# Performance work log

Measured on AMD Instinct MI355X. Metric: run time of the kernel, lower is better.

The kernel has to match this reference:

```python
import jax, jax.numpy as jnp
import numpy as np
from jax import lax

NUM_PATCHES = 64   # FPS sample count K
PATCH_SIZE = 32    # KNN neighbors per patch


def setup_inputs() -> dict:
    key = jax.random.key(0)
    points = jax.random.normal(key, (16, 65536, 3), dtype=jnp.float32)
    return {"points": points}


def _fps(xyz, K):
    """Iterative farthest point sampling. xyz: [B,N,3] -> idx [B,K].
    Deterministic start at index 0 (reference for random_start_point)."""
    B, N, _ = xyz.shape
    start = jnp.zeros((B,), dtype=jnp.int32)
    min_d0 = jnp.full((B, N), jnp.finfo(xyz.dtype).max, xyz.dtype)

    def step(carry, _):
        min_d, last = carry
        last_pt = jnp.take_along_axis(xyz, last[:, None, None], axis=1)  # [B,1,3]
        d = jnp.sum((xyz - last_pt) ** 2, axis=-1)                       # [B,N]
        min_d = jnp.minimum(min_d, d)
        nxt = jnp.argmax(min_d, axis=1).astype(jnp.int32)
        return (min_d, nxt), last

    (_, _), idxs = lax.scan(step, (min_d0, start), None, length=K)  # [K,B]
    return jnp.transpose(idxs)  # [B,K]


def _knn_idx(centers, pts, K):
    """K nearest neighbors (sorted ascending by distance). centers [B,P,3], pts [B,N,3]."""
    c2 = jnp.sum(centers * centers, -1)[:, :, None]                 # [B,P,1]
    p2 = jnp.sum(pts * pts, -1)[:, None, :]                         # [B,1,N]
    d2 = c2 + p2 - 2.0 * jnp.einsum('bpc,bnc->bpn', centers, pts)   # [B,P,N]
    _, idx = lax.top_k(-d2, K)                                      # sorted nearest-first
    return idx


def reference(points):
    xyz = points[..., :3]
    fps_idx = _fps(xyz, NUM_PATCHES)                                  # [B,P]
    centers = jnp.take_along_axis(xyz, fps_idx[..., None], axis=1)    # [B,P,3]
    idx = _knn_idx(centers, xyz, PATCH_SIZE)                          # [B,P,K]
    patches = jax.vmap(lambda p, i: p[i])(points, idx)                # [B,P,K,C]
    patches = patches.at[..., :3].add(-centers[:, :, None, :])        # center xyz part
    return patches, centers
```

## Files before the change

### kernel.cpp

```cpp
#include <hip/hip_runtime.h>
#include <float.h>

#define BATCH 16
#define NPTS  65536
#define NP    64
#define PS    32
#define SLICES 8
#define SLICE_PTS (NPTS / SLICES)
#define CAP   192


__device__ __forceinline__ unsigned long long enc64(double d) {
    unsigned long long u = (unsigned long long)__double_as_longlong(d);
    return u ^ ((u >> 63) ? 0xFFFFFFFFFFFFFFFFull : 0x8000000000000000ull);
}
__device__ __forceinline__ unsigned enc32(float f) {
    unsigned u = __float_as_uint(f);
    return u ^ ((u >> 31) ? 0xFFFFFFFFu : 0x80000000u);
}
__device__ __forceinline__ float dec32(unsigned e) {
    unsigned u = (e & 0x80000000u) ? (e ^ 0x80000000u) : ~e;
    return __uint_as_float(u);
}

#define SENT 0xFFFFFFFFFFFFFFFFull

__global__ __launch_bounds__(256, 2)
void fps_kernel(const float* __restrict__ pts,
                float* __restrict__ centers,
                unsigned long long* __restrict__ slots)
{
#pragma clang fp contract(off)
    const int b  = blockIdx.x & 15;
    const int wg = blockIdx.x >> 4;
    const int t  = threadIdx.x;
    const float* __restrict__ P = pts + (size_t)b * NPTS * 3;

    float x[16], y[16], z[16];
    double md[16];
    const int gi0 = wg * 4096 + t;
#pragma unroll
    for (int k = 0; k < 16; ++k) {
        int i = gi0 + (k << 8);
        x[k] = P[3*i+0]; y[k] = P[3*i+1]; z[k] = P[3*i+2];
        md[k] = DBL_MAX;
    }

    double cx = (double)P[0], cy = (double)P[1], cz = (double)P[2];
    if (wg == 0 && t == 0) {
        float* c0 = centers + b * (NP*3);
        c0[0] = P[0]; c0[1] = P[1]; c0[2] = P[2];
    }

    __shared__ unsigned long long wbest[4];
    __shared__ unsigned long long skey[16];

    unsigned long long* slot_it = slots + (size_t)b * 63 * 16;

    for (int it = 0; it < NP - 1; ++it) {
        double bd = -1.0; int bi = 0;
#pragma unroll
        for (int k = 0; k < 16; ++k) {
            double dx = (double)x[k] - cx;
            double dy = (double)y[k] - cy;
            double dz = (double)z[k] - cz;
            double d  = (dx*dx + dy*dy) + dz*dz;
            double m  = fmin(md[k], d);
            md[k] = m;
            if (m > bd) { bd = m; bi = gi0 + (k << 8); }
        }
        unsigned long long db  = (unsigned long long)__double_as_longlong(bd);
        unsigned long long key = 0x8000000000000000ull
                               | (db & 0xFFFFFFFFFFFF0000ull)
                               | (unsigned long long)((~bi) & 0xFFFF);
#pragma unroll
        for (int off = 32; off > 0; off >>= 1) {
            unsigned long long o = __shfl_xor(key, off, 64);
            if (o > key) key = o;
        }
        if ((t & 63) == 0) wbest[t >> 6] = key;
        __syncthreads();
        if (t == 0) {
            unsigned long long k0 = wbest[0];
            if (wbest[1] > k0) k0 = wbest[1];
            if (wbest[2] > k0) k0 = wbest[2];
            if (wbest[3] > k0) k0 = wbest[3];
            __hip_atomic_store(slot_it + wg, k0, __ATOMIC_RELAXED, __HIP_MEMORY_SCOPE_AGENT);
        }
        if (t < 16) {
            unsigned long long v;
            v = __hip_atomic_load(slot_it + t, __ATOMIC_RELAXED, __HIP_MEMORY_SCOPE_AGENT);
            while (v == 0) {
                __builtin_amdgcn_s_sleep(1);
                v = __hip_atomic_load(slot_it + t, __ATOMIC_RELAXED, __HIP_MEMORY_SCOPE_AGENT);
            }
            skey[t] = v;
        }
        __syncthreads();
        unsigned long long bk = skey[0];
#pragma unroll
        for (int j = 1; j < 16; ++j) if (skey[j] > bk) bk = skey[j];
        int sel = (int)((~bk) & 0xFFFFull);
        cx = (double)P[3*sel+0]; cy = (double)P[3*sel+1]; cz = (double)P[3*sel+2];
        if (wg == 0 && t == 0) {
            float* c = centers + b*(NP*3) + (it+1)*3;
            c[0] = P[3*sel+0]; c[1] = P[3*sel+1]; c[2] = P[3*sel+2];
        }
        slot_it += 16;
    }
}

__global__ __launch_bounds__(256, 4)
void knn_pass(const float* __restrict__ pts,
              const float* __restrict__ centers,
              unsigned long long* __restrict__ gkeys)
{
    const int t    = threadIdx.x;
    const int lane = t & 63;
    const int wid  = t >> 6;
    const int b    = blockIdx.x & 15;
    const int w    = (blockIdx.x >> 4) & 15;
    const int s    = blockIdx.x >> 8;
    const float* __restrict__ P = pts + (size_t)b * NPTS * 3;
    const int sbase = s * SLICE_PTS;
    const float4* __restrict__ P4 = (const float4*)(P + 3 * sbase);

    float cxf[4], cyf[4], czf[4], c2f[4];
#pragma unroll
    for (int g = 0; g < 4; ++g) {
        int c = b * NP + w * 4 + g;
        cxf[g] = centers[3*c+0]; cyf[g] = centers[3*c+1]; czf[g] = centers[3*c+2];
        c2f[g] = cxf[g]*cxf[g] + cyf[g]*cyf[g] + czf[g]*czf[g];
    }

    __shared__ unsigned pool[4][512];
    __shared__ float    theta4[4];
    __shared__ int      cnt4[4];
    __shared__ unsigned idxbuf[4][CAP];

    float s0[4], s1[4];
#pragma unroll
    for (int g = 0; g < 4; ++g) { s0[g] = FLT_MAX; s1[g] = FLT_MAX; }
    {
        float4 A = P4[3*t], B = P4[3*t+1], C = P4[3*t+2];
        for (int k = 0; k < SLICE_PTS/1024; ++k) {
            int vb = ((k+1) & 7)*768 + 3*t;
            float4 An = P4[vb], Bn = P4[vb+1], Cn = P4[vb+2];
            float qx[4] = {A.x, A.w, B.z, C.y};
            float qy[4] = {A.y, B.x, B.w, C.z};
            float qz[4] = {A.z, B.y, C.x, C.w};
#pragma unroll
            for (int j = 0; j < 4; ++j) {
                float px = qx[j], py = qy[j], pz = qz[j];
                float p2 = px*px + py*py + pz*pz;
#pragma unroll
                for (int g = 0; g < 4; ++g) {
                    float dt = cxf[g]*px + cyf[g]*py + czf[g]*pz;
                    float d2 = (c2f[g] + p2) - 2.0f*dt;
                    float mx = fmaxf(d2, s0[g]);
                    s0[g] = fminf(s0[g], d2);
                    s1[g] = fminf(s1[g], mx);
                }
            }
            A = An; B = Bn; C = Cn;
        }
    }
#pragma unroll
    for (int g = 0; g < 4; ++g) {
        pool[g][t]       = enc32(s0[g]);
        pool[g][256 + t] = enc32(s1[g]);
    }
    if (t < 4) cnt4[t] = 0;
    __syncthreads();

    {
        const int g = wid;
        unsigned e[8];
#pragma unroll
        for (int j = 0; j < 8; ++j) e[j] = pool[g][lane * 8 + j];
        unsigned ans = 0;
        for (int bit = 31; bit >= 0; --bit) {
            unsigned test = ans | ((1u << bit) - 1u);
            int cnt = 0;
#pragma unroll
            for (int j = 0; j < 8; ++j)
                cnt += (int)__popcll(__ballot(e[j] <= test));
            if (cnt < 32) ans |= (1u << bit);
        }
        if (lane == 0) theta4[g] = dec32(ans) + 4.0e-3f;
    }
    __syncthreads();
    float th[4];
#pragma unroll
    for (int g = 0; g < 4; ++g) th[g] = theta4[g];

    {
        float4 A = P4[3*t], B = P4[3*t+1], C = P4[3*t+2];
        for (int k = 0; k < SLICE_PTS/1024; ++k) {
            int vb = ((k+1) & 7)*768 + 3*t;
            float4 An = P4[vb], Bn = P4[vb+1], Cn = P4[vb+2];
            float qx[4] = {A.x, A.w, B.z, C.y};
            float qy[4] = {A.y, B.x, B.w, C.z};
            float qz[4] = {A.z, B.y, C.x, C.w};
            int ib = sbase + (k << 10) + (t << 2);
#pragma unroll
            for (int j = 0; j < 4; ++j) {
                float px = qx[j], py = qy[j], pz = qz[j];
                float p2 = px*px + py*py + pz*pz;
#pragma unroll
                for (int g = 0; g < 4; ++g) {
                    float dt = cxf[g]*px + cyf[g]*py + czf[g]*pz;
                    float d2 = (c2f[g] + p2) - 2.0f*dt;
                    if (d2 <= th[g]) {
                        int pos = atomicAdd(&cnt4[g], 1);
                        if (pos < CAP) idxbuf[g][pos] = (unsigned)(ib + j);
                    }
                }
            }
            A = An; B = Bn; C = Cn;
        }
    }
    __syncthreads();

    {
        const int g = wid;
        int n = cnt4[g]; if (n > CAP) n = CAP;
        double cxd, cyd, czd, c2d;
        {
#pragma clang fp contract(off)
            cxd = (double)cxf[g]; cyd = (double)cyf[g]; czd = (double)czf[g];
            c2d = (cxd*cxd + cyd*cyd) + czd*czd;
        }
        unsigned long long rg[3];
#pragma unroll
        for (int j = 0; j < 3; ++j) {
            int p_ = lane + 64*j;
            if (p_ < n) {
                unsigned i = idxbuf[g][p_];
                double d2x;
                {
#pragma clang fp contract(off)
                    double px_ = (double)P[3*i+0];
                    double py_ = (double)P[3*i+1];
                    double pz_ = (double)P[3*i+2];
                    double p2_ = (px_*px_ + py_*py_) + pz_*pz_;
                    double dt_ = (cxd*px_ + cyd*py_) + czd*pz_;
                    d2x = (c2d + p2_) - 2.0*dt_;
                }
                rg[j] = (enc64(d2x) & 0xFFFFFFFFFFFF0000ull)
                      | (unsigned long long)(i & 0xFFFF);
            } else rg[j] = SENT;
        }
        const int c = b * NP + w * 4 + g;
        unsigned long long okey = SENT;
        for (int r = 0; r < PS; ++r) {
            unsigned long long mn = rg[0]; int mp = 0;
            if (rg[1] < mn) { mn = rg[1]; mp = 1; }
            if (rg[2] < mn) { mn = rg[2]; mp = 2; }
            unsigned long long wm = mn;
#pragma unroll
            for (int off = 32; off > 0; off >>= 1) {
                unsigned long long o = __shfl_xor(wm, off, 64);
                if (o < wm) wm = o;
            }
            if (wm == mn) {
                if (mp == 0) rg[0] = SENT;
                else if (mp == 1) rg[1] = SENT;
                else rg[2] = SENT;
            }
            if (lane == r) okey = wm;
        }
        if (lane < PS)
            gkeys[((size_t)c * SLICES + s) * PS + lane] = okey;
    }
}

__global__ __launch_bounds__(256, 4)
void knn_merge(const float* __restrict__ pts,
               const float* __restrict__ centers,
               const unsigned long long* __restrict__ gkeys,
               float* __restrict__ patches)
{
    const int lane = threadIdx.x & 63;
    const int wid  = threadIdx.x >> 6;
    const int b    = blockIdx.x & 15;
    const int grp  = blockIdx.x >> 4;
    const int c    = b * NP + grp * 4 + wid;
    const float* __restrict__ P = pts + (size_t)b * NPTS * 3;

    unsigned long long rg[4];
#pragma unroll
    for (int j = 0; j < 4; ++j)
        rg[j] = gkeys[(size_t)c * (SLICES*PS) + j*64 + lane];

    unsigned long long okey = SENT;
    for (int r = 0; r < PS; ++r) {
        unsigned long long mn = rg[0]; int mp = 0;
        if (rg[1] < mn) { mn = rg[1]; mp = 1; }
        if (rg[2] < mn) { mn = rg[2]; mp = 2; }
        if (rg[3] < mn) { mn = rg[3]; mp = 3; }
        unsigned long long wm = mn;
#pragma unroll
        for (int off = 32; off > 0; off >>= 1) {
            unsigned long long o = __shfl_xor(wm, off, 64);
            if (o < wm) wm = o;
        }
        if (wm == mn) {
            if (mp == 0) rg[0] = SENT;
            else if (mp == 1) rg[1] = SENT;
            else if (mp == 2) rg[2] = SENT;
            else rg[3] = SENT;
        }
        if (lane == r) okey = wm;
    }

    const float cx = centers[3*c+0], cy = centers[3*c+1], cz = centers[3*c+2];
    if (lane < PS) {
        int i = (int)(okey & 0xFFFFull);
        float* o = patches + (((size_t)c * PS) + lane) * 3;
        o[0] = P[3*i+0] - cx;
        o[1] = P[3*i+1] - cy;
        o[2] = P[3*i+2] - cz;
    }
}

extern "C" void kernel_launch(void* const* d_in, const int* in_sizes, int n_in,
                              void* d_out, int out_size, void* d_ws, size_t ws_size,
                              hipStream_t stream)
{
    const float* pts = (const float*)d_in[0];
    float* out      = (float*)d_out;
    float* patches  = out;
    float* centers  = out + (size_t)BATCH*NP*PS*3;

    unsigned long long* slots = (unsigned long long*)d_ws;
    unsigned long long* gkeys = (unsigned long long*)((char*)d_ws + 131072);

    (void)hipMemsetAsync(d_ws, 0, (size_t)BATCH * 63 * 16 * sizeof(unsigned long long), stream);
    fps_kernel<<<dim3(256), dim3(256), 0, stream>>>(pts, centers, slots);
    knn_pass<<<dim3(2048), dim3(256), 0, stream>>>(pts, centers, gkeys);
    knn_merge<<<dim3(256), dim3(256), 0, stream>>>(pts, centers, gkeys, patches);
}
```

Measured before the change: 260.1 us.

## Speculatively select two FPS points per iteration when the runner-up provably stays farthest

Each FPS round now tracks the top two candidates per thread, wave, block and grid. If the distance between the runner-up and the new center is at least the runner-up's own min-distance, the runner-up must be the next farthest point, so both are accepted and the next round updates min-distances against two centers. This cuts the number of grid-wide spin-wait synchronisations, which dominate the serial FPS loop. In exchange each round does extra top-2 reduction and a second slot exchange, and the acceptance test relies on truncated 48-bit distance keys, which may affect exactness on ties.

```diff
diff --git a/kernel.cpp b/kernel.cpp
--- a/kernel.cpp
+++ b/kernel.cpp
@@ -47,18 +47,21 @@
     }
 
     double cx = (double)P[0], cy = (double)P[1], cz = (double)P[2];
+    double qx = 0.0, qy = 0.0, qz = 0.0;
+    bool dual = false;
     if (wg == 0 && t == 0) {
         float* c0 = centers + b * (NP*3);
         c0[0] = P[0]; c0[1] = P[1]; c0[2] = P[2];
     }
 
-    __shared__ unsigned long long wbest[4];
-    __shared__ unsigned long long skey[16];
-
-    unsigned long long* slot_it = slots + (size_t)b * 63 * 16;
-
-    for (int it = 0; it < NP - 1; ++it) {
-        double bd = -1.0; int bi = 0;
+    __shared__ unsigned long long wk1[4], wk2[4];
+    __shared__ unsigned long long sk1[16], sk2[16];
+
+    unsigned long long* slot_it = slots + (size_t)b * 63 * 32;
+
+    int nsel = 1;
+    while (nsel < NP) {
+        double bd1 = -1.0, bd2 = -1.0; int bi1 = 0, bi2 = 0;
 #pragma unroll
         for (int k = 0; k < 16; ++k) {
             double dx = (double)x[k] - cx;
@@ -66,47 +69,99 @@
             double dz = (double)z[k] - cz;
             double d  = (dx*dx + dy*dy) + dz*dz;
             double m  = fmin(md[k], d);
+            if (dual) {
+                double ex = (double)x[k] - qx;
+                double ey = (double)y[k] - qy;
+                double ez = (double)z[k] - qz;
+                double e  = (ex*ex + ey*ey) + ez*ez;
+                m = fmin(m, e);
+            }
             md[k] = m;
-            if (m > bd) { bd = m; bi = gi0 + (k << 8); }
-        }
-        unsigned long long db  = (unsigned long long)__double_as_longlong(bd);
-        unsigned long long key = 0x8000000000000000ull
-                               | (db & 0xFFFFFFFFFFFF0000ull)
-                               | (unsigned long long)((~bi) & 0xFFFF);
+            int i = gi0 + (k << 8);
+            if (m > bd1)      { bd2 = bd1; bi2 = bi1; bd1 = m; bi1 = i; }
+            else if (m > bd2) { bd2 = m;  bi2 = i; }
+        }
+        unsigned long long k1 = 0x8000000000000000ull
+            | ((unsigned long long)__double_as_longlong(bd1) & 0xFFFFFFFFFFFF0000ull)
+            | (unsigned long long)((~bi1) & 0xFFFF);
+        unsigned long long k2 = 0x8000000000000000ull
+            | ((unsigned long long)__double_as_longlong(bd2) & 0xFFFFFFFFFFFF0000ull)
+            | (unsigned long long)((~bi2) & 0xFFFF);
+
+        unsigned long long K1 = k1;
 #pragma unroll
         for (int off = 32; off > 0; off >>= 1) {
-            unsigned long long o = __shfl_xor(key, off, 64);
-            if (o > key) key = o;
-        }
-        if ((t & 63) == 0) wbest[t >> 6] = key;
+            unsigned long long o = __shfl_xor(K1, off, 64);
+            if (o > K1) K1 = o;
+        }
+        unsigned long long K2 = (k1 == K1) ? k2 : k1;
+#pragma unroll
+        for (int off = 32; off > 0; off >>= 1) {
+            unsigned long long o = __shfl_xor(K2, off, 64);
+            if (o > K2) K2 = o;
+        }
+        if ((t & 63) == 0) { wk1[t >> 6] = K1; wk2[t >> 6] = K2; }
         __syncthreads();
         if (t == 0) {
-            unsigned long long k0 = wbest[0];
-            if (wbest[1] > k0) k0 = wbest[1];
-            if (wbest[2] > k0) k0 = wbest[2];
-            if (wbest[3] > k0) k0 = wbest[3];
-            __hip_atomic_store(slot_it + wg, k0, __ATOMIC_RELAXED, __HIP_MEMORY_SCOPE_AGENT);
+            unsigned long long B1 = 0, B2 = 0;
+#pragma unroll
+            for (int j = 0; j < 4; ++j) {
+                unsigned long long a = wk1[j];
+                if (a > B1) { B2 = B1; B1 = a; } else if (a > B2) B2 = a;
+                unsigned long long c = wk2[j];
+                if (c > B1) { B2 = B1; B1 = c; } else if (c > B2) B2 = c;
+            }
+            __hip_atomic_store(slot_it + wg*2 + 0, B1, __ATOMIC_RELAXED, __HIP_MEMORY_SCOPE_AGENT);
+            __hip_atomic_store(slot_it + wg*2 + 1, B2, __ATOMIC_RELAXED, __HIP_MEMORY_SCOPE_AGENT);
         }
         if (t < 16) {
-            unsigned long long v;
-            v = __hip_atomic_load(slot_it + t, __ATOMIC_RELAXED, __HIP_MEMORY_SCOPE_AGENT);
-            while (v == 0) {
+            unsigned long long v1, v2;
+            v1 = __hip_atomic_load(slot_it + t*2 + 0, __ATOMIC_RELAXED, __HIP_MEMORY_SCOPE_AGENT);
+            while (v1 == 0) {
                 __builtin_amdgcn_s_sleep(1);
-                v = __hip_atomic_load(slot_it + t, __ATOMIC_RELAXED, __HIP_MEMORY_SCOPE_AGENT);
-            }
-            skey[t] = v;
+                v1 = __hip_atomic_load(slot_it + t*2 + 0, __ATOMIC_RELAXED, __HIP_MEMORY_SCOPE_AGENT);
+            }
+            v2 = __hip_atomic_load(slot_it + t*2 + 1, __ATOMIC_RELAXED, __HIP_MEMORY_SCOPE_AGENT);
+            while (v2 == 0) {
+                __builtin_amdgcn_s_sleep(1);
+                v2 = __hip_atomic_load(slot_it + t*2 + 1, __ATOMIC_RELAXED, __HIP_MEMORY_SCOPE_AGENT);
+            }
+            sk1[t] = v1; sk2[t] = v2;
         }
         __syncthreads();
-        unsigned long long bk = skey[0];
-#pragma unroll
-        for (int j = 1; j < 16; ++j) if (skey[j] > bk) bk = skey[j];
-        int sel = (int)((~bk) & 0xFFFFull);
-        cx = (double)P[3*sel+0]; cy = (double)P[3*sel+1]; cz = (double)P[3*sel+2];
+        unsigned long long B1 = 0, B2 = 0;
+#pragma unroll
+        for (int j = 0; j < 16; ++j) {
+            unsigned long long a = sk1[j];
+            if (a > B1) { B2 = B1; B1 = a; } else if (a > B2) B2 = a;
+            unsigned long long c = sk2[j];
+            if (c > B1) { B2 = B1; B1 = c; } else if (c > B2) B2 = c;
+        }
+        int sel1 = (int)((~B1) & 0xFFFFull);
+        cx = (double)P[3*sel1+0]; cy = (double)P[3*sel1+1]; cz = (double)P[3*sel1+2];
         if (wg == 0 && t == 0) {
-            float* c = centers + b*(NP*3) + (it+1)*3;
-            c[0] = P[3*sel+0]; c[1] = P[3*sel+1]; c[2] = P[3*sel+2];
-        }
-        slot_it += 16;
+            float* c = centers + b*(NP*3) + nsel*3;
+            c[0] = P[3*sel1+0]; c[1] = P[3*sel1+1]; c[2] = P[3*sel1+2];
+        }
+        dual = false;
+        if (nsel + 2 <= NP) {
+            int sel2 = (int)((~B2) & 0xFFFFull);
+            qx = (double)P[3*sel2+0]; qy = (double)P[3*sel2+1]; qz = (double)P[3*sel2+2];
+            double gx = qx - cx, gy = qy - cy, gz = qz - cz;
+            double d21 = (gx*gx + gy*gy) + gz*gz;
+            unsigned long long encd = (unsigned long long)__double_as_longlong(d21)
+                                    | 0x8000000000000000ull;
+            unsigned long long ub = (B2 & 0xFFFFFFFFFFFF0000ull) + 0x10000ull;
+            if (encd >= ub) {
+                dual = true;
+                if (wg == 0 && t == 0) {
+                    float* c = centers + b*(NP*3) + (nsel+1)*3;
+                    c[0] = P[3*sel2+0]; c[1] = P[3*sel2+1]; c[2] = P[3*sel2+2];
+                }
+            }
+        }
+        nsel += dual ? 2 : 1;
+        slot_it += 32;
     }
 }
 
@@ -334,9 +389,9 @@
     float* centers  = out + (size_t)BATCH*NP*PS*3;
 
     unsigned long long* slots = (unsigned long long*)d_ws;
-    unsigned long long* gkeys = (unsigned long long*)((char*)d_ws + 131072);
-
-    (void)hipMemsetAsync(d_ws, 0, (size_t)BATCH * 63 * 16 * sizeof(unsigned long long), stream);
+    unsigned long long* gkeys = (unsigned long long*)((char*)d_ws + 262144);
+
+    (void)hipMemsetAsync(d_ws, 0, (size_t)BATCH * 63 * 16 * 2 * sizeof(unsigned long long), stream);
     fps_kernel<<<dim3(256), dim3(256), 0, stream>>>(pts, centers, slots);
     knn_pass<<<dim3(2048), dim3(256), 0, stream>>>(pts, centers, gkeys);
     knn_merge<<<dim3(256), dim3(256), 0, stream>>>(pts, centers, gkeys, patches);
```

Measured after the change: 510.2 us. 96.2% more time.

## Fold distance into FMAs with med3 tracking and use rank-based top-32 selection

Applied to the files above, without the earlier changes.

The hot distance loops now use precomputed -2*center coefficients, so each squared distance is a chain of three FMAs plus one add. The running second-minimum is updated with a single fmed3 instruction instead of a max/min pair. The 32-round wave-shuffle selection of the nearest candidates is replaced by writing keys to shared memory, which is unioned with the pool buffer. Each lane counts its key's rank and scatters the key directly to its output slot. Output slots beyond the candidate count are no longer filled with a sentinel, and this relies on the threshold always admitting at least 32 candidates.

```diff
diff --git a/kernel.cpp b/kernel.cpp
--- a/kernel.cpp
+++ b/kernel.cpp
@@ -125,15 +125,20 @@
     const int sbase = s * SLICE_PTS;
     const float4* __restrict__ P4 = (const float4*)(P + 3 * sbase);
 
-    float cxf[4], cyf[4], czf[4], c2f[4];
+    float m2x[4], m2y[4], m2z[4], c2f[4];
 #pragma unroll
     for (int g = 0; g < 4; ++g) {
         int c = b * NP + w * 4 + g;
-        cxf[g] = centers[3*c+0]; cyf[g] = centers[3*c+1]; czf[g] = centers[3*c+2];
-        c2f[g] = cxf[g]*cxf[g] + cyf[g]*cyf[g] + czf[g]*czf[g];
-    }
-
-    __shared__ unsigned pool[4][512];
+        float cx = centers[3*c+0], cy = centers[3*c+1], cz = centers[3*c+2];
+        c2f[g] = cx*cx + cy*cy + cz*cz;
+        m2x[g] = -2.0f*cx; m2y[g] = -2.0f*cy; m2z[g] = -2.0f*cz;
+    }
+
+    union PoolKeys {
+        unsigned pool[4][512];
+        unsigned long long keys[4][CAP];
+    };
+    __shared__ PoolKeys pk;
     __shared__ float    theta4[4];
     __shared__ int      cnt4[4];
     __shared__ unsigned idxbuf[4][CAP];
@@ -155,11 +160,9 @@
                 float p2 = px*px + py*py + pz*pz;
 #pragma unroll
                 for (int g = 0; g < 4; ++g) {
-                    float dt = cxf[g]*px + cyf[g]*py + czf[g]*pz;
-                    float d2 = (c2f[g] + p2) - 2.0f*dt;
-                    float mx = fmaxf(d2, s0[g]);
+                    float d2 = fmaf(m2x[g], px, fmaf(m2y[g], py, fmaf(m2z[g], pz, c2f[g]))) + p2;
+                    s1[g] = __builtin_amdgcn_fmed3f(s0[g], s1[g], d2);
                     s0[g] = fminf(s0[g], d2);
-                    s1[g] = fminf(s1[g], mx);
                 }
             }
             A = An; B = Bn; C = Cn;
@@ -167,8 +170,8 @@
     }
 #pragma unroll
     for (int g = 0; g < 4; ++g) {
-        pool[g][t]       = enc32(s0[g]);
-        pool[g][256 + t] = enc32(s1[g]);
+        pk.pool[g][t]       = enc32(s0[g]);
+        pk.pool[g][256 + t] = enc32(s1[g]);
     }
     if (t < 4) cnt4[t] = 0;
     __syncthreads();
@@ -177,7 +180,7 @@
         const int g = wid;
         unsigned e[8];
 #pragma unroll
-        for (int j = 0; j < 8; ++j) e[j] = pool[g][lane * 8 + j];
+        for (int j = 0; j < 8; ++j) e[j] = pk.pool[g][lane * 8 + j];
         unsigned ans = 0;
         for (int bit = 31; bit >= 0; --bit) {
             unsigned test = ans | ((1u << bit) - 1u);
@@ -209,8 +212,7 @@
                 float p2 = px*px + py*py + pz*pz;
 #pragma unroll
                 for (int g = 0; g < 4; ++g) {
-                    float dt = cxf[g]*px + cyf[g]*py + czf[g]*pz;
-                    float d2 = (c2f[g] + p2) - 2.0f*dt;
+                    float d2 = fmaf(m2x[g], px, fmaf(m2y[g], py, fmaf(m2z[g], pz, c2f[g]))) + p2;
                     if (d2 <= th[g]) {
                         int pos = atomicAdd(&cnt4[g], 1);
                         if (pos < CAP) idxbuf[g][pos] = (unsigned)(ib + j);
@@ -228,7 +230,7 @@
         double cxd, cyd, czd, c2d;
         {
 #pragma clang fp contract(off)
-            cxd = (double)cxf[g]; cyd = (double)cyf[g]; czd = (double)czf[g];
+            cxd = -0.5*(double)m2x[g]; cyd = -0.5*(double)m2y[g]; czd = -0.5*(double)m2z[g];
             c2d = (cxd*cxd + cyd*cyd) + czd*czd;
         }
         unsigned long long rg[3];
@@ -249,29 +251,21 @@
                 }
                 rg[j] = (enc64(d2x) & 0xFFFFFFFFFFFF0000ull)
                       | (unsigned long long)(i & 0xFFFF);
+                pk.keys[g][p_] = rg[j];
             } else rg[j] = SENT;
         }
         const int c = b * NP + w * 4 + g;
-        unsigned long long okey = SENT;
-        for (int r = 0; r < PS; ++r) {
-            unsigned long long mn = rg[0]; int mp = 0;
-            if (rg[1] < mn) { mn = rg[1]; mp = 1; }
-            if (rg[2] < mn) { mn = rg[2]; mp = 2; }
-            unsigned long long wm = mn;
-#pragma unroll
-            for (int off = 32; off > 0; off >>= 1) {
-                unsigned long long o = __shfl_xor(wm, off, 64);
-                if (o < wm) wm = o;
-            }
-            if (wm == mn) {
-                if (mp == 0) rg[0] = SENT;
-                else if (mp == 1) rg[1] = SENT;
-                else rg[2] = SENT;
-            }
-            if (lane == r) okey = wm;
-        }
-        if (lane < PS)
-            gkeys[((size_t)c * SLICES + s) * PS + lane] = okey;
+        int rank0 = 0, rank1 = 0, rank2 = 0;
+        for (int p = 0; p < n; ++p) {
+            unsigned long long kj = pk.keys[g][p];
+            rank0 += (kj < rg[0]);
+            rank1 += (kj < rg[1]);
+            rank2 += (kj < rg[2]);
+        }
+        unsigned long long* gout = gkeys + ((size_t)c * SLICES + s) * PS;
+        if (lane       < n && rank0 < PS) gout[rank0] = rg[0];
+        if (lane + 64  < n && rank1 < PS) gout[rank1] = rg[1];
+        if (lane + 128 < n && rank2 < PS) gout[rank2] = rg[2];
     }
 }
 
```

Result: faster. 224.0 us (-13.9%).
